# Optimization experiments

Hardware: AMD Instinct MI355X
Metric: run time of the kernel (lower is better)

Reference implementation:

```python
import jax, jax.numpy as jnp
import numpy as np

N_QUBITS = 9
N_LAYERS = 4
EPS = 1e-5


def _apply_ry(state, wire, theta):
    # state: [N, 2**n] real; theta: [N] or scalar
    n = N_QUBITS
    N = state.shape[0]
    left, right = 2 ** wire, 2 ** (n - 1 - wire)
    s = state.reshape(N, left, 2, right)
    th = jnp.broadcast_to(jnp.asarray(theta, state.dtype), (N,))[:, None, None]
    c, si = jnp.cos(th / 2), jnp.sin(th / 2)
    a, b = s[:, :, 0, :], s[:, :, 1, :]
    out = jnp.stack([c * a - si * b, si * a + c * b], axis=2)
    return out.reshape(N, -1)


def _apply_cnot(state, ctrl, tgt):
    n = N_QUBITS
    N = state.shape[0]
    s = state.reshape((N,) + (2,) * n)
    ca, ta = ctrl + 1, tgt + 1
    sub = jnp.take(s, 1, axis=ca)          # control == 1 slice
    ta2 = ta - 1 if ta > ca else ta
    sub = jnp.flip(sub, axis=ta2)          # X on target
    idx = [slice(None)] * (n + 1)
    idx[ca] = 1
    s = s.at[tuple(idx)].set(sub)
    return s.reshape(N, -1)


def quantum_layer(inputs, q_weights):
    # inputs: [N, n_qubits] angles; q_weights: [n_layers, n_qubits]
    N = inputs.shape[0]
    state = jnp.zeros((N, 2 ** N_QUBITS), inputs.dtype).at[:, 0].set(1.0)
    for i in range(N_QUBITS):
        state = _apply_ry(state, i, inputs[:, i])
    for j in range(N_LAYERS):
        for i in range(N_QUBITS):
            state = _apply_cnot(state, i, (i + 1) % N_QUBITS)
        for i in range(N_QUBITS):
            state = _apply_ry(state, i, q_weights[j, i])
    probs = (state * state).reshape((N,) + (2,) * N_QUBITS)
    zs = []
    for i in range(N_QUBITS):
        axes = tuple(a for a in range(1, N_QUBITS + 1) if a != i + 1)
        p = probs.sum(axes)                # [N, 2]
        zs.append(p[:, 0] - p[:, 1])
    return jnp.stack(zs, axis=1)           # [N, n_qubits]


def _bn(x):
    mu = x.mean((0, 2, 3), keepdims=True)
    var = x.var((0, 2, 3), keepdims=True)
    return (x - mu) * jax.lax.rsqrt(var + EPS)


def _maxpool(x, kh, kw):
    return jax.lax.reduce_window(x, -jnp.inf, jax.lax.max,
                                 (1, 1, kh, kw), (1, 1, kh, kw), 'VALID')


def _conv(x, w):
    return jax.lax.conv_general_dilated(x, w, (1, 1), 'VALID',
                                        dimension_numbers=('NCHW', 'OIHW', 'NCHW'))


def _forward(x, w_conv1, w_conv2, w_conv3, q_weights, fc_w, fc_b):
    h = jax.nn.elu(_bn(_conv(x, w_conv1)))
    h = jnp.pad(h, ((0, 0), (0, 0), (0, 1), (16, 17)))     # ZeroPad2d(16,17,0,1)
    h = _maxpool(jax.nn.elu(_bn(_conv(h, w_conv2))), 2, 4)
    h = jnp.pad(h, ((0, 0), (0, 0), (4, 3), (2, 1)))       # ZeroPad2d(2,1,4,3)
    h = _maxpool(jax.nn.elu(_bn(_conv(h, w_conv3))), 2, 4)
    B, C = h.shape[0], h.shape[1]
    feats = h.reshape(B, C, -1)                            # [B, 32, 9]
    q = quantum_layer(feats.reshape(B * C, N_QUBITS), q_weights)
    q = q.reshape(B, C * N_QUBITS)                         # channel-major concat
    return q @ fc_w.T + fc_b


def setup_inputs() -> dict:
    key = jax.random.key(0)
    ks = jax.random.split(key, 7)
    return {
        'x': jax.random.normal(ks[0], (1024, 1, 4, 216), jnp.float32),
        'w_conv1': jax.random.normal(ks[1], (16, 1, 1, 64), jnp.float32) * 0.05,
        'w_conv2': jax.random.normal(ks[2], (32, 16, 2, 32), jnp.float32) * 0.05,
        'w_conv3': jax.random.normal(ks[3], (32, 32, 8, 4), jnp.float32) * 0.05,
        'q_weights': jax.random.uniform(ks[4], (N_LAYERS, N_QUBITS), jnp.float32, 0.0, 2 * np.pi),
        'fc_w': jax.random.normal(ks[5], (5, 32 * N_QUBITS), jnp.float32) * 0.05,
        'fc_b': jnp.zeros((5,), jnp.float32),
    }


def reference(x, w_conv1, w_conv2, w_conv3, q_weights, fc_w, fc_b):
    return _forward(x, w_conv1, w_conv2, w_conv3, q_weights, fc_w, fc_b)
```

## Files before the change

### kernel.cpp

```cpp
#include <hip/hip_runtime.h>
#include <math.h>

#define NB 1024
#define C1 16
#define H1 4
#define W1 153
#define WX 216
#define K1 64
#define C2 32
#define H2 4
#define W2 155
#define W192 192
#define PW2 38
#define C3 32
#define W3 38

typedef short short4v __attribute__((ext_vector_type(4)));
typedef short short8 __attribute__((ext_vector_type(8)));
typedef float f32x16 __attribute__((ext_vector_type(16)));

#define OFF_OUT1     0
#define OFF_A1H      10027008
#define OFF_A1L      16318464
#define OFF_W2PH     22609920
#define OFF_W2PL     22626304
#define OFF_W3PH     22642688
#define OFF_W3PL     22659072
#define OFF_UH       22675456
#define OFF_UL       22806528
#define OFF_POOL2RAW 22937600
#define OFF_A2H      25427968
#define OFF_A2L      27787264
#define OFF_FEATSRAW 30146560
#define OFF_QO       30441472
#define OFF_PART1    30736384
#define OFF_PART2    30867456
#define OFF_PART3    30998528
#define OFF_STATS1   31031296
#define OFF_STATS2   31031328
#define OFF_STATS3   31031392

__device__ __forceinline__ float eluf(float x){ return x > 0.f ? x : expm1f(x); }

__device__ __forceinline__ ushort bf16h(float x){
  unsigned u = __float_as_uint(x);
  unsigned r = u + 0x7fffu + ((u >> 16) & 1u);
  return (ushort)(r >> 16);
}
__device__ __forceinline__ float bf16f(ushort h){ return __uint_as_float(((unsigned)h) << 16); }

__device__ __forceinline__ short8 cat8(short4v a, short4v b){
  return __builtin_shufflevector(a, b, 0,1,2,3,4,5,6,7);
}

__global__ __launch_bounds__(256) void k_conv1s(const float* __restrict__ x,
                                                const float* __restrict__ w1,
                                                float* __restrict__ out1,
                                                float* __restrict__ part1){
  __shared__ float xr[4][WX];
  __shared__ float wl[C1*K1];
  int n = blockIdx.x, tid = threadIdx.x;
  for (int i = tid; i < 4*WX; i += 256) xr[i/WX][i%WX] = x[(size_t)n*4*WX + i];
  for (int i = tid; i < C1*K1; i += 256) wl[i] = w1[i];
  __syncthreads();
  int h = tid >> 6, lane = tid & 63;
  float acc[16][3];
  #pragma unroll
  for (int c = 0; c < 16; ++c){ acc[c][0]=0.f; acc[c][1]=0.f; acc[c][2]=0.f; }
  bool v2 = (lane + 128) < W1;
  for (int k = 0; k < 64; ++k){
    float x0 = xr[h][lane + k];
    float x1 = xr[h][lane + 64 + k];
    float x2 = v2 ? xr[h][lane + 128 + k] : 0.f;
    #pragma unroll
    for (int c = 0; c < 16; ++c){
      float wk = wl[c*64 + k];
      acc[c][0] += wk*x0; acc[c][1] += wk*x1; acc[c][2] += wk*x2;
    }
  }
  float ss[16], sq[16];
  #pragma unroll
  for (int c = 0; c < 16; ++c){
    float* ob = out1 + (((size_t)(n*16 + c)*4 + h))*W1;
    ob[lane] = acc[c][0];
    ob[lane + 64] = acc[c][1];
    if (v2) ob[lane + 128] = acc[c][2];
    ss[c] = acc[c][0] + acc[c][1] + acc[c][2];
    sq[c] = acc[c][0]*acc[c][0] + acc[c][1]*acc[c][1] + acc[c][2]*acc[c][2];
  }
  #pragma unroll
  for (int m = 1; m < 64; m <<= 1){
    #pragma unroll
    for (int c = 0; c < 16; ++c){ ss[c] += __shfl_xor(ss[c], m); sq[c] += __shfl_xor(sq[c], m); }
  }
  if (lane == 0){
    #pragma unroll
    for (int c = 0; c < 16; ++c){
      part1[((size_t)(n*4 + h)*16 + c)*2]     = ss[c];
      part1[((size_t)(n*4 + h)*16 + c)*2 + 1] = sq[c];
    }
  }
}

__global__ __launch_bounds__(256) void k_stats_finP(const float* __restrict__ part,
                                                    float* __restrict__ stats,
                                                    int C, int nblk, float inv){
  __shared__ float rs[256], rq[256];
  int c = blockIdx.x;
  float s = 0.f, q = 0.f;
  for (int b = threadIdx.x; b < nblk; b += 256){
    s += part[((size_t)b*C + c)*2];
    q += part[((size_t)b*C + c)*2 + 1];
  }
  rs[threadIdx.x] = s; rq[threadIdx.x] = q; __syncthreads();
  for (int st = 128; st > 0; st >>= 1){
    if (threadIdx.x < st){ rs[threadIdx.x] += rs[threadIdx.x+st]; rq[threadIdx.x] += rq[threadIdx.x+st]; }
    __syncthreads();
  }
  if (threadIdx.x == 0){
    float mean = rs[0]*inv;
    float var  = rq[0]*inv - mean*mean;
    stats[c*2]   = mean;
    stats[c*2+1] = rsqrtf(var + 1e-5f);
  }
}

__global__ __launch_bounds__(256) void k_bnelu1(const float* __restrict__ out1,
                                                const float* __restrict__ stats,
                                                ushort* __restrict__ a1h, ushort* __restrict__ a1l){
  __shared__ float xf[2448];
  __shared__ float st[32];
  int b = blockIdx.x;
  int n = b >> 2, h = b & 3;
  int tid = threadIdx.x;
  if (tid < 32) st[tid] = stats[tid];
  for (int i = tid; i < 2448; i += 256){
    int ci = i / 153, w = i - ci*153;
    xf[i] = out1[((size_t)(n*16 + ci)*4 + h)*W1 + w];
  }
  __syncthreads();
  for (int i = tid; i < 3072; i += 256){
    int w = i >> 4, ci = i & 15;
    float v = 0.f;
    int ws = w - 16;
    if ((unsigned)ws < (unsigned)W1){
      float xx = xf[ci*153 + ws];
      v = eluf((xx - st[ci*2])*st[ci*2+1]);
    }
    int ciS = ci ^ (((w >> 2) & 3) << 2);
    size_t o = (size_t)b*3072 + w*16 + ciS;
    ushort hs = bf16h(v);
    a1h[o] = hs;
    a1l[o] = bf16h(v - bf16f(hs));
  }
}

__global__ void k_cvtw(const float* __restrict__ w2, const float* __restrict__ w3,
                       ushort* __restrict__ w2ph, ushort* __restrict__ w2pl,
                       ushort* __restrict__ w3ph, ushort* __restrict__ w3pl){
  int idx = blockIdx.x*256 + threadIdx.x;
  if (idx < 32768){
    int ci = idx & 15; int co = (idx >> 4) & 31; int rk = idx >> 9;
    int r = rk >> 5, kw = rk & 31;
    float v = w2[((size_t)(co*16 + ci)*2 + r)*32 + kw];
    ushort hs = bf16h(v); float hf = bf16f(hs);
    w2ph[idx] = hs; w2pl[idx] = bf16h(v - hf);
  } else {
    int j = idx - 32768;
    int ci = j & 31; int co = (j >> 5) & 31; int rk = j >> 10;
    int r = rk >> 2, kw = rk & 3;
    float v = w3[((size_t)(co*32 + ci)*8 + r)*4 + kw];
    ushort hs = bf16h(v); float hf = bf16f(hs);
    w3ph[j] = hs; w3pl[j] = bf16h(v - hf);
  }
}

template<int HG>
__global__ __launch_bounds__(256, 3) void k_conv2fT(const ushort* __restrict__ a1h,
                                                    const ushort* __restrict__ a1l,
                                                    const ushort* __restrict__ w2ph,
                                                    const ushort* __restrict__ w2pl,
                                                    float* __restrict__ pool2raw,
                                                    float* __restrict__ part2){
  constexpr int NR = HG ? 2 : 3;
  __shared__ __align__(16) ushort s_hi[NR*3072];
  __shared__ __align__(16) ushort s_lo[NR*3072];
  __shared__ float statW[4][32][2];
  int n = blockIdx.x;
  int tid = threadIdx.x;
  {
    const float4* gh = (const float4*)(a1h + ((size_t)n*4 + 2*HG)*3072);
    const float4* gl = (const float4*)(a1l + ((size_t)n*4 + 2*HG)*3072);
    float4* dh = (float4*)s_hi;
    float4* dl = (float4*)s_lo;
    #pragma unroll
    for (int i = 0; i < NR*384; i += 256){
      int k = i + tid;
      if (k < NR*384){ dh[k] = gh[k]; dl[k] = gl[k]; }
    }
  }
  __syncthreads();
  int wv = tid >> 6, lane = tid & 63;
  int l5 = lane >> 5, l31 = lane & 31;
  int ps = (wv + n) & 3;
  int p0 = (ps == 0) ? 0 : (ps + 1);
  bool two = (ps == 0);
  int e4 = l5*4;

  f32x16 acc[2][2];
  #pragma unroll
  for (int lh = 0; lh < 2; ++lh)
    #pragma unroll
    for (int p = 0; p < 2; ++p)
      #pragma unroll
      for (int e = 0; e < 16; ++e) acc[lh][p][e] = 0.f;

  for (int kw = 0; kw < 32; ++kw){
    short8 Ah[2], Al[2];
    #pragma unroll
    for (int r = 0; r < 2; ++r){
      int widx = ((r*32 + kw)*32 + l31)*16 + e4;
      Ah[r] = cat8(*(const short4v*)(w2ph + widx), *(const short4v*)(w2ph + widx + 8));
      Al[r] = cat8(*(const short4v*)(w2pl + widx), *(const short4v*)(w2pl + widx + 8));
    }
    short8 bh[NR][2], bl[NR][2];
    #pragma unroll
    for (int j = 0; j < NR; ++j){
      #pragma unroll
      for (int p = 0; p < 2; ++p){
        int pf = p0 + p; pf = (pf > 4) ? 4 : pf;
        int pos = pf*32 + l31 + kw;
        int sw = ((pos >> 2) & 3) << 2;
        int off0 = j*3072 + pos*16 + (e4 ^ sw);
        int off1 = off0 ^ 8;
        bh[j][p] = cat8(*(const short4v*)(s_hi + off0), *(const short4v*)(s_hi + off1));
        bl[j][p] = cat8(*(const short4v*)(s_lo + off0), *(const short4v*)(s_lo + off1));
      }
    }
    #pragma unroll
    for (int lh = 0; lh < 2; ++lh){
      #pragma unroll
      for (int r = 0; r < 2; ++r){
        if (lh + r < NR){
          acc[lh][0] = __builtin_amdgcn_mfma_f32_32x32x16_bf16(Ah[r], bh[lh+r][0], acc[lh][0], 0, 0, 0);
          acc[lh][0] = __builtin_amdgcn_mfma_f32_32x32x16_bf16(Ah[r], bl[lh+r][0], acc[lh][0], 0, 0, 0);
          acc[lh][0] = __builtin_amdgcn_mfma_f32_32x32x16_bf16(Al[r], bh[lh+r][0], acc[lh][0], 0, 0, 0);
        }
      }
    }
    if (two){
      #pragma unroll
      for (int lh = 0; lh < 2; ++lh){
        #pragma unroll
        for (int r = 0; r < 2; ++r){
          if (lh + r < NR){
            acc[lh][1] = __builtin_amdgcn_mfma_f32_32x32x16_bf16(Ah[r], bh[lh+r][1], acc[lh][1], 0, 0, 0);
            acc[lh][1] = __builtin_amdgcn_mfma_f32_32x32x16_bf16(Ah[r], bl[lh+r][1], acc[lh][1], 0, 0, 0);
            acc[lh][1] = __builtin_amdgcn_mfma_f32_32x32x16_bf16(Al[r], bh[lh+r][1], acc[lh][1], 0, 0, 0);
          }
        }
      }
    }
  }

  int np = two ? 2 : 1;
  {
    float sreg[16], qreg[16];
    #pragma unroll
    for (int e = 0; e < 16; ++e){ sreg[e] = 0.f; qreg[e] = 0.f; }
    #pragma unroll
    for (int lh = 0; lh < 2; ++lh){
      #pragma unroll
      for (int p = 0; p < 2; ++p){
        bool pv = (p < np) && (((p0 + p) < 4) || (l31 < 27));
        #pragma unroll
        for (int e = 0; e < 16; ++e){
          float v = pv ? acc[lh][p][e] : 0.f;
          sreg[e] += v; qreg[e] += v*v;
        }
      }
    }
    #pragma unroll
    for (int m = 1; m < 32; m <<= 1){
      #pragma unroll
      for (int e = 0; e < 16; ++e){
        sreg[e] += __shfl_xor(sreg[e], m);
        qreg[e] += __shfl_xor(qreg[e], m);
      }
    }
    if (l31 == 0){
      #pragma unroll
      for (int e = 0; e < 16; ++e){
        int co = (e & 3) + ((e >> 2) << 3) + (l5 << 2);
        statW[ps][co][0] = sreg[e];
        statW[ps][co][1] = qreg[e];
      }
    }
  }
  #pragma unroll
  for (int p = 0; p < 2; ++p){
    if (p < np){
      #pragma unroll
      for (int e = 0; e < 16; ++e){
        float m0 = fmaxf(acc[0][p][e], acc[1][p][e]);
        float v1 = fmaxf(m0, __shfl_xor(m0, 1));
        float v2m = fmaxf(v1, __shfl_xor(v1, 2));
        int pw = (p0 + p)*8 + (l31 >> 2);
        if ((l31 & 3) == 0 && pw < PW2){
          int co = (e & 3) + ((e >> 2) << 3) + (l5 << 2);
          pool2raw[(((size_t)n*2 + HG)*32 + co)*PW2 + pw] = v2m;
        }
      }
    }
  }
  __syncthreads();
  if (tid < 32){
    float s = statW[0][tid][0] + statW[1][tid][0] + statW[2][tid][0] + statW[3][tid][0];
    float q = statW[0][tid][1] + statW[1][tid][1] + statW[2][tid][1] + statW[3][tid][1];
    part2[(((size_t)n*2 + HG)*32 + tid)*2]     = s;
    part2[(((size_t)n*2 + HG)*32 + tid)*2 + 1] = q;
  }
}

__global__ __launch_bounds__(256) void k_bn2(const float* __restrict__ pool2raw,
                                             const float* __restrict__ stats,
                                             ushort* __restrict__ a2h, ushort* __restrict__ a2l){
  __shared__ float xf[1216];
  __shared__ float st[64];
  int b = blockIdx.x;
  int tid = threadIdx.x;
  if (tid < 64) st[tid] = stats[tid];
  for (int i = tid; i < 1216; i += 256) xf[i] = pool2raw[(size_t)b*1216 + i];
  __syncthreads();
  for (int i = tid; i < 2304; i += 256){
    int w = i >> 5, ci = i & 31;
    float v = 0.f;
    int pw = w - 2;
    if ((unsigned)pw < (unsigned)PW2)
      v = eluf((xf[ci*38 + pw] - st[ci*2])*st[ci*2+1]);
    int ciS = ci ^ (((w >> 1) & 7) << 2);
    size_t o = (size_t)b*2304 + w*32 + ciS;
    ushort hs = bf16h(v);
    a2h[o] = hs; a2l[o] = bf16h(v - bf16f(hs));
  }
}

__global__ __launch_bounds__(256, 2) void k_conv3f(const ushort* __restrict__ a2h,
                                                   const ushort* __restrict__ a2l,
                                                   const ushort* __restrict__ w3ph,
                                                   const ushort* __restrict__ w3pl,
                                                   float* __restrict__ featsraw,
                                                   float* __restrict__ part3){
  __shared__ __align__(16) ushort s3h[9216];
  __shared__ __align__(16) ushort s3l[9216];
  __shared__ float poolL3[4][32][12];
  __shared__ float statL3[4][32][2];
  int nb = blockIdx.x;
  int tid = threadIdx.x;
  {
    const float4* gh = (const float4*)(a2h + (size_t)nb*9216);
    const float4* gl = (const float4*)(a2l + (size_t)nb*9216);
    float4* dh = (float4*)s3h;
    float4* dl = (float4*)s3l;
    for (int i = tid; i < 1152; i += 256){ dh[i] = gh[i]; dl[i] = gl[i]; }
  }
  __syncthreads();
  int wave = tid >> 6, lane = tid & 63;
  int nh = wave >> 1, h = wave & 1;
  int l5 = lane >> 5, l31 = lane & 31;

  f32x16 acc[2];
  #pragma unroll
  for (int p = 0; p < 2; ++p)
    #pragma unroll
    for (int e = 0; e < 16; ++e) acc[p][e] = 0.f;

  #pragma unroll
  for (int ri = 0; ri < 2; ++ri){
    int r = (h == 0) ? (4 + ri) : (3 + ri);
    int rbase = (nh*2 + ri)*72*32;
    #pragma unroll
    for (int kw = 0; kw < 4; ++kw){
      #pragma unroll
      for (int ch = 0; ch < 2; ++ch){
        int widx = ((r*4 + kw)*32 + l31)*32 + ch*16 + l5*4;
        short8 Ah = cat8(*(const short4v*)(w3ph + widx), *(const short4v*)(w3ph + widx + 8));
        short8 Al = cat8(*(const short4v*)(w3pl + widx), *(const short4v*)(w3pl + widx + 8));
        short8 Bh[2], Bl[2];
        #pragma unroll
        for (int p = 0; p < 2; ++p){
          int pos = p*32 + l31 + kw;
          int sw = ((pos >> 1) & 7) << 2;
          int s0 = ch*16 + l5*4;
          int off0 = rbase + pos*32 + (s0 ^ sw);
          int off1 = rbase + pos*32 + ((s0 + 8) ^ sw);
          Bh[p] = cat8(*(const short4v*)(s3h + off0), *(const short4v*)(s3h + off1));
          Bl[p] = cat8(*(const short4v*)(s3l + off0), *(const short4v*)(s3l + off1));
        }
        #pragma unroll
        for (int p = 0; p < 2; ++p) acc[p] = __builtin_amdgcn_mfma_f32_32x32x16_bf16(Ah, Bh[p], acc[p], 0, 0, 0);
        #pragma unroll
        for (int p = 0; p < 2; ++p) acc[p] = __builtin_amdgcn_mfma_f32_32x32x16_bf16(Ah, Bl[p], acc[p], 0, 0, 0);
        #pragma unroll
        for (int p = 0; p < 2; ++p) acc[p] = __builtin_amdgcn_mfma_f32_32x32x16_bf16(Al, Bh[p], acc[p], 0, 0, 0);
      }
    }
  }

  {
    float sreg[16], qreg[16];
    #pragma unroll
    for (int e = 0; e < 16; ++e){ sreg[e] = 0.f; qreg[e] = 0.f; }
    #pragma unroll
    for (int p = 0; p < 2; ++p){
      bool pv = (p == 0) || (l31 < 6);
      #pragma unroll
      for (int e = 0; e < 16; ++e){
        float v = pv ? acc[p][e] : 0.f;
        sreg[e] += v; qreg[e] += v*v;
      }
    }
    #pragma unroll
    for (int m = 1; m < 32; m <<= 1){
      #pragma unroll
      for (int e = 0; e < 16; ++e){
        sreg[e] += __shfl_xor(sreg[e], m);
        qreg[e] += __shfl_xor(qreg[e], m);
      }
    }
    if (l31 == 0){
      #pragma unroll
      for (int e = 0; e < 16; ++e){
        int co = (e & 3) + ((e >> 2) << 3) + (l5 << 2);
        statL3[wave][co][0] = sreg[e];
        statL3[wave][co][1] = qreg[e];
      }
    }
  }
  #pragma unroll
  for (int p = 0; p < 2; ++p){
    #pragma unroll
    for (int e = 0; e < 16; ++e){
      float v = acc[p][e];
      float v1 = fmaxf(v, __shfl_xor(v, 1));
      float v2m = fmaxf(v1, __shfl_xor(v1, 2));
      int pw = p*8 + (l31 >> 2);
      if ((l31 & 3) == 0 && pw < 9){
        int co = (e & 3) + ((e >> 2) << 3) + (l5 << 2);
        poolL3[wave][co][pw] = v2m;
      }
    }
  }
  __syncthreads();
  for (int i = tid; i < 2*32*9; i += 256){
    int pw = i % 9; int t = i / 9; int co = t & 31; int nh2 = t >> 5;
    float v = fmaxf(poolL3[nh2*2][co][pw], poolL3[nh2*2+1][co][pw]);
    featsraw[((size_t)(nb*2 + nh2)*32 + co)*9 + pw] = v;
  }
  if (tid < 32){
    float s = 0.f, q = 0.f;
    #pragma unroll
    for (int wv = 0; wv < 4; ++wv){ s += statL3[wv][tid][0]; q += statL3[wv][tid][1]; }
    part3[((size_t)nb*32 + tid)*2]     = s;
    part3[((size_t)nb*32 + tid)*2 + 1] = q;
  }
}

__global__ __launch_bounds__(256) void k_buildU(const float* __restrict__ qw,
                                                ushort* __restrict__ Uh, ushort* __restrict__ Ul){
  __shared__ float wt[36][2];
  int tid = threadIdx.x;
  if (tid < 36){ float s, c; sincosf(qw[tid]*0.5f, &s, &c); wt[tid][0] = c; wt[tid][1] = s; }
  __syncthreads();
  int wid = tid >> 6, lane = tid & 63;
  int k = blockIdx.x*4 + wid;
  float v[8];
  #pragma unroll
  for (int r = 0; r < 8; ++r) v[r] = (lane*8 + r == k) ? 1.f : 0.f;

  for (int j = 0; j < 4; ++j){
    #pragma unroll
    for (int i = 0; i < 5; ++i){
      int cm = 32>>i, tm = 16>>i;
      bool flip = (lane & cm) != 0;
      #pragma unroll
      for (int r = 0; r < 8; ++r){
        float w = __shfl_xor(v[r], tm);
        v[r] = flip ? w : v[r];
      }
    }
    { bool flip = (lane & 1) != 0;
      #pragma unroll
      for (int r = 0; r < 4; ++r){ float a = v[r], bb = v[r+4]; v[r] = flip?bb:a; v[r+4] = flip?a:bb; } }
    { float t = v[4]; v[4] = v[6]; v[6] = t; t = v[5]; v[5] = v[7]; v[7] = t; }
    { float t = v[2]; v[2] = v[3]; v[3] = t; t = v[6]; v[6] = v[7]; v[7] = t; }
    #pragma unroll
    for (int r = 1; r < 8; r += 2) v[r] = __shfl_xor(v[r], 32);

    #pragma unroll
    for (int i = 0; i < 6; ++i){
      float c = wt[j*9+i][0], s = wt[j*9+i][1];
      int m = 32>>i;
      float sg = (lane & m) ? s : -s;
      #pragma unroll
      for (int r = 0; r < 8; ++r){
        float w = __shfl_xor(v[r], m);
        v[r] = c*v[r] + sg*w;
      }
    }
    { float c = wt[j*9+6][0], s = wt[j*9+6][1];
      #pragma unroll
      for (int r = 0; r < 4; ++r){ float a = v[r], bb = v[r+4]; v[r] = c*a - s*bb; v[r+4] = s*a + c*bb; } }
    { float c = wt[j*9+7][0], s = wt[j*9+7][1]; float a, bb;
      a=v[0]; bb=v[2]; v[0]=c*a-s*bb; v[2]=s*a+c*bb;
      a=v[1]; bb=v[3]; v[1]=c*a-s*bb; v[3]=s*a+c*bb;
      a=v[4]; bb=v[6]; v[4]=c*a-s*bb; v[6]=s*a+c*bb;
      a=v[5]; bb=v[7]; v[5]=c*a-s*bb; v[7]=s*a+c*bb; }
    { float c = wt[j*9+8][0], s = wt[j*9+8][1]; float a, bb;
      a=v[0]; bb=v[1]; v[0]=c*a-s*bb; v[1]=s*a+c*bb;
      a=v[2]; bb=v[3]; v[2]=c*a-s*bb; v[3]=s*a+c*bb;
      a=v[4]; bb=v[5]; v[4]=c*a-s*bb; v[5]=s*a+c*bb;
      a=v[6]; bb=v[7]; v[6]=c*a-s*bb; v[7]=s*a+c*bb; }
  }
  #pragma unroll
  for (int r = 0; r < 8; ++r){
    int s = lane*8 + r;
    int mf = s >> 5, r31 = s & 31;
    int addr = (((k >> 4)*16 + mf)*32 + r31)*16 + (k & 15);
    float f = v[r];
    ushort hi = bf16h(f);
    Uh[addr] = hi;
    Ul[addr] = bf16h(f - bf16f(hi));
  }
}

__global__ __launch_bounds__(256, 1) void k_qgemm(const float* __restrict__ featsraw,
                                                  const float* __restrict__ stats,
                                                  const ushort* __restrict__ Uh,
                                                  const ushort* __restrict__ Ul,
                                                  float* __restrict__ qo){
  __shared__ __align__(16) ushort BhL[32768];
  __shared__ __align__(16) ushort BlL[32768];
  __shared__ float angL[576];
  __shared__ float zred[4][64][9];
  int nb = blockIdx.x;
  int tid = threadIdx.x;
  for (int t = tid; t < 576; t += 256){
    float vr = featsraw[(size_t)nb*576 + t];
    int c = (t/9) & 31;
    angL[t] = 0.5f * eluf((vr - stats[c*2])*stats[c*2+1]);
  }
  __syncthreads();
  {
    int sm = tid >> 2, q = tid & 3;
    float tc[9], ts[9];
    #pragma unroll
    for (int i = 0; i < 9; ++i) sincosf(angL[sm*9 + i], &ts[i], &tc[i]);
    float Pc = ((q & 2) ? ts[0] : tc[0]) * ((q & 1) ? ts[1] : tc[1]);
    int swz = (sm >> 2) & 3;
    short4v* bh4 = (short4v*)BhL;
    short4v* bl4 = (short4v*)BlL;
    int j = 0;
    #pragma unroll
    for (int b2 = 0; b2 < 2; ++b2){ float p2 = Pc*(b2 ? ts[2] : tc[2]);
    #pragma unroll
    for (int b3 = 0; b3 < 2; ++b3){ float p3 = p2*(b3 ? ts[3] : tc[3]);
    #pragma unroll
    for (int b4 = 0; b4 < 2; ++b4){ float p4 = p3*(b4 ? ts[4] : tc[4]);
    #pragma unroll
    for (int b5 = 0; b5 < 2; ++b5){ float p5 = p4*(b5 ? ts[5] : tc[5]);
    #pragma unroll
    for (int b6 = 0; b6 < 2; ++b6){ float p6 = p5*(b6 ? ts[6] : tc[6]);
      float a0 = p6*tc[7]*tc[8];
      float a1 = p6*tc[7]*ts[8];
      float a2 = p6*ts[7]*tc[8];
      float a3 = p6*ts[7]*ts[8];
      ushort h0 = bf16h(a0), h1 = bf16h(a1), h2 = bf16h(a2), h3 = bf16h(a3);
      short4v hv; hv[0]=(short)h0; hv[1]=(short)h1; hv[2]=(short)h2; hv[3]=(short)h3;
      short4v lv; lv[0]=(short)bf16h(a0 - bf16f(h0)); lv[1]=(short)bf16h(a1 - bf16f(h1));
                  lv[2]=(short)bf16h(a2 - bf16f(h2)); lv[3]=(short)bf16h(a3 - bf16f(h3));
      int kk = q*128 + j;
      int kstep = kk >> 4;
      int g = (kk >> 2) & 3;
      int idx4 = (kstep*64 + sm)*4 + (g ^ swz);
      bh4[idx4] = hv; bl4[idx4] = lv;
      j += 4;
    }}}}}
  }
  __syncthreads();
  int wv = tid >> 6, lane = tid & 63, l5 = lane >> 5, l31 = lane & 31;
  f32x16 acc[4][2];
  #pragma unroll
  for (int jj = 0; jj < 4; ++jj)
    #pragma unroll
    for (int nf = 0; nf < 2; ++nf)
      #pragma unroll
      for (int e = 0; e < 16; ++e) acc[jj][nf][e] = 0.f;

  for (int kstep = 0; kstep < 32; ++kstep){
    short8 Bh[2], Bl[2];
    #pragma unroll
    for (int nf = 0; nf < 2; ++nf){
      int sm = nf*32 + l31;
      int base = (kstep*64 + sm)*16;
      int sz = ((sm >> 2) & 3) << 2;
      int e0 = (l5*4) ^ sz;
      int e1 = (l5*4 + 8) ^ sz;
      Bh[nf] = cat8(*(const short4v*)(BhL + base + e0), *(const short4v*)(BhL + base + e1));
      Bl[nf] = cat8(*(const short4v*)(BlL + base + e0), *(const short4v*)(BlL + base + e1));
    }
    #pragma unroll
    for (int jj = 0; jj < 4; ++jj){
      int mf = wv*4 + jj;
      const ushort* ah = Uh + ((kstep*16 + mf)*32 + l31)*16 + l5*4;
      const ushort* al = Ul + ((kstep*16 + mf)*32 + l31)*16 + l5*4;
      short8 Ah = cat8(*(const short4v*)ah, *(const short4v*)(ah + 8));
      short8 Al = cat8(*(const short4v*)al, *(const short4v*)(al + 8));
      acc[jj][0] = __builtin_amdgcn_mfma_f32_32x32x16_bf16(Ah, Bh[0], acc[jj][0], 0, 0, 0);
      acc[jj][1] = __builtin_amdgcn_mfma_f32_32x32x16_bf16(Ah, Bh[1], acc[jj][1], 0, 0, 0);
      acc[jj][0] = __builtin_amdgcn_mfma_f32_32x32x16_bf16(Ah, Bl[0], acc[jj][0], 0, 0, 0);
      acc[jj][1] = __builtin_amdgcn_mfma_f32_32x32x16_bf16(Ah, Bl[1], acc[jj][1], 0, 0, 0);
      acc[jj][0] = __builtin_amdgcn_mfma_f32_32x32x16_bf16(Al, Bh[0], acc[jj][0], 0, 0, 0);
      acc[jj][1] = __builtin_amdgcn_mfma_f32_32x32x16_bf16(Al, Bh[1], acc[jj][1], 0, 0, 0);
    }
  }
  float zz[2][9];
  #pragma unroll
  for (int nf = 0; nf < 2; ++nf)
    #pragma unroll
    for (int i = 0; i < 9; ++i) zz[nf][i] = 0.f;
  #pragma unroll
  for (int jj = 0; jj < 4; ++jj){
    int mf = wv*4 + jj;
    float sg0 = (mf & 8) ? -1.f : 1.f;
    float sg1 = (mf & 4) ? -1.f : 1.f;
    float sg2 = (mf & 2) ? -1.f : 1.f;
    float sg3 = (mf & 1) ? -1.f : 1.f;
    #pragma unroll
    for (int nf = 0; nf < 2; ++nf){
      float psum = 0.f, z4 = 0.f, z5 = 0.f, z7 = 0.f, z8 = 0.f;
      #pragma unroll
      for (int e = 0; e < 16; ++e){
        float qv = acc[jj][nf][e]*acc[jj][nf][e];
        psum += qv;
        z4 += ((e >> 3) & 1) ? -qv : qv;
        z5 += ((e >> 2) & 1) ? -qv : qv;
        z7 += ((e >> 1) & 1) ? -qv : qv;
        z8 += (e & 1) ? -qv : qv;
      }
      zz[nf][0] += sg0*psum; zz[nf][1] += sg1*psum;
      zz[nf][2] += sg2*psum; zz[nf][3] += sg3*psum;
      zz[nf][4] += z4; zz[nf][5] += z5;
      zz[nf][6] += l5 ? -psum : psum;
      zz[nf][7] += z7; zz[nf][8] += z8;
    }
  }
  #pragma unroll
  for (int nf = 0; nf < 2; ++nf)
    #pragma unroll
    for (int i = 0; i < 9; ++i) zz[nf][i] += __shfl_xor(zz[nf][i], 32);
  if (l5 == 0){
    #pragma unroll
    for (int nf = 0; nf < 2; ++nf)
      #pragma unroll
      for (int i = 0; i < 9; ++i) zred[wv][nf*32 + l31][i] = zz[nf][i];
  }
  __syncthreads();
  for (int t = tid; t < 576; t += 256){
    int sm = t / 9, i = t - sm*9;
    float s = zred[0][sm][i] + zred[1][sm][i] + zred[2][sm][i] + zred[3][sm][i];
    qo[(size_t)(nb*64 + sm)*9 + i] = s;
  }
}

__global__ void k_fc(const float* __restrict__ q, const float* __restrict__ fw,
                     const float* __restrict__ fb, float* __restrict__ out){
  int idx = blockIdx.x*256 + threadIdx.x;
  if (idx >= NB*5) return;
  int b = idx / 5, o = idx - b*5;
  const float* qr = q + (size_t)b*288;
  const float* wr = fw + (size_t)o*288;
  float s = 0.f;
  for (int j = 0; j < 288; ++j) s += qr[j]*wr[j];
  out[idx] = s + fb[o];
}

extern "C" void kernel_launch(void* const* d_in, const int* in_sizes, int n_in,
                              void* d_out, int out_size, void* d_ws, size_t ws_size,
                              hipStream_t stream){
  const float* x  = (const float*)d_in[0];
  const float* w1 = (const float*)d_in[1];
  const float* w2 = (const float*)d_in[2];
  const float* w3 = (const float*)d_in[3];
  const float* qw = (const float*)d_in[4];
  const float* fw = (const float*)d_in[5];
  const float* fb = (const float*)d_in[6];
  float* out = (float*)d_out;
  float* W = (float*)d_ws;

  float*  out1   = W + OFF_OUT1;
  ushort* a1h    = (ushort*)(W + OFF_A1H);
  ushort* a1l    = (ushort*)(W + OFF_A1L);
  ushort* w2ph   = (ushort*)(W + OFF_W2PH);
  ushort* w2pl   = (ushort*)(W + OFF_W2PL);
  ushort* w3ph   = (ushort*)(W + OFF_W3PH);
  ushort* w3pl   = (ushort*)(W + OFF_W3PL);
  ushort* uH     = (ushort*)(W + OFF_UH);
  ushort* uL     = (ushort*)(W + OFF_UL);
  float*  pool2raw = W + OFF_POOL2RAW;
  ushort* a2h    = (ushort*)(W + OFF_A2H);
  ushort* a2l    = (ushort*)(W + OFF_A2L);
  float*  featsraw = W + OFF_FEATSRAW;
  float*  qo     = W + OFF_QO;
  float*  part1  = W + OFF_PART1;
  float*  part2  = W + OFF_PART2;
  float*  part3  = W + OFF_PART3;
  float*  stats1 = W + OFF_STATS1;
  float*  stats2 = W + OFF_STATS2;
  float*  stats3 = W + OFF_STATS3;

  k_conv1s<<<NB, 256, 0, stream>>>(x, w1, out1, part1);
  k_stats_finP<<<16, 256, 0, stream>>>(part1, stats1, 16, NB*4, 1.f/((float)NB*H1*W1));
  k_bnelu1<<<NB*4, 256, 0, stream>>>(out1, stats1, a1h, a1l);
  k_cvtw<<<256, 256, 0, stream>>>(w2, w3, w2ph, w2pl, w3ph, w3pl);
  k_buildU<<<128, 256, 0, stream>>>(qw, uH, uL);
  k_conv2fT<0><<<NB, 256, 0, stream>>>(a1h, a1l, w2ph, w2pl, pool2raw, part2);
  k_conv2fT<1><<<NB, 256, 0, stream>>>(a1h, a1l, w2ph, w2pl, pool2raw, part2);
  k_stats_finP<<<32, 256, 0, stream>>>(part2, stats2, 32, NB*2, 1.f/((float)NB*H2*W2));
  k_bn2<<<NB*2, 256, 0, stream>>>(pool2raw, stats2, a2h, a2l);
  k_conv3f<<<NB/2, 256, 0, stream>>>(a2h, a2l, w3ph, w3pl, featsraw, part3);
  k_stats_finP<<<32, 256, 0, stream>>>(part3, stats3, 32, NB/2, 1.f/((float)NB*2*W3));
  k_qgemm<<<NB/2, 256, 0, stream>>>(featsraw, stats3, uH, uL, qo);
  k_fc<<<20, 256, 0, stream>>>(qo, fw, fb, out);
}
```

Baseline: 337.9 us.

## Split conv2 work across five waves, one position tile per wave

The conv2 kernel moves from 4 waves per block, where one wave handled two position tiles, to 5 waves of 320 threads, each handling exactly one 32-wide position tile. This removes the imbalance in which one wave did double the MFMA work while the others idled. Launch bounds change to (320,5), and the per-wave stats array grows to five slots. The cost is more waves per block and a possible change in register budget and occupancy.

Result: faster. 328.2 us (-2.9%).

```diff
diff --git a/kernel.cpp b/kernel.cpp
--- a/kernel.cpp
+++ b/kernel.cpp
@@ -176,7 +176,7 @@
 }
 
 template<int HG>
-__global__ __launch_bounds__(256, 3) void k_conv2fT(const ushort* __restrict__ a1h,
+__global__ __launch_bounds__(320, 5) void k_conv2f5(const ushort* __restrict__ a1h,
                                                     const ushort* __restrict__ a1l,
                                                     const ushort* __restrict__ w2ph,
                                                     const ushort* __restrict__ w2pl,
@@ -185,7 +185,7 @@
   constexpr int NR = HG ? 2 : 3;
   __shared__ __align__(16) ushort s_hi[NR*3072];
   __shared__ __align__(16) ushort s_lo[NR*3072];
-  __shared__ float statW[4][32][2];
+  __shared__ float statW[5][32][2];
   int n = blockIdx.x;
   int tid = threadIdx.x;
   {
@@ -193,27 +193,17 @@
     const float4* gl = (const float4*)(a1l + ((size_t)n*4 + 2*HG)*3072);
     float4* dh = (float4*)s_hi;
     float4* dl = (float4*)s_lo;
-    #pragma unroll
-    for (int i = 0; i < NR*384; i += 256){
-      int k = i + tid;
-      if (k < NR*384){ dh[k] = gh[k]; dl[k] = gl[k]; }
-    }
-  }
-  __syncthreads();
-  int wv = tid >> 6, lane = tid & 63;
+    for (int i = tid; i < NR*384; i += 320){ dh[i] = gh[i]; dl[i] = gl[i]; }
+  }
+  __syncthreads();
+  int wave = tid >> 6, lane = tid & 63;
   int l5 = lane >> 5, l31 = lane & 31;
-  int ps = (wv + n) & 3;
-  int p0 = (ps == 0) ? 0 : (ps + 1);
-  bool two = (ps == 0);
+  int p = wave + (n % 5); p = (p >= 5) ? p - 5 : p;
   int e4 = l5*4;
 
-  f32x16 acc[2][2];
-  #pragma unroll
-  for (int lh = 0; lh < 2; ++lh)
-    #pragma unroll
-    for (int p = 0; p < 2; ++p)
-      #pragma unroll
-      for (int e = 0; e < 16; ++e) acc[lh][p][e] = 0.f;
+  f32x16 acc0, acc1;
+  #pragma unroll
+  for (int e = 0; e < 16; ++e){ acc0[e] = 0.f; acc1[e] = 0.f; }
 
   for (int kw = 0; kw < 32; ++kw){
     short8 Ah[2], Al[2];
@@ -223,62 +213,41 @@
       Ah[r] = cat8(*(const short4v*)(w2ph + widx), *(const short4v*)(w2ph + widx + 8));
       Al[r] = cat8(*(const short4v*)(w2pl + widx), *(const short4v*)(w2pl + widx + 8));
     }
-    short8 bh[NR][2], bl[NR][2];
+    short8 bh[NR], bl[NR];
+    int pos = p*32 + l31 + kw;
+    int sw = ((pos >> 2) & 3) << 2;
+    int o0 = pos*16 + (e4 ^ sw);
     #pragma unroll
     for (int j = 0; j < NR; ++j){
-      #pragma unroll
-      for (int p = 0; p < 2; ++p){
-        int pf = p0 + p; pf = (pf > 4) ? 4 : pf;
-        int pos = pf*32 + l31 + kw;
-        int sw = ((pos >> 2) & 3) << 2;
-        int off0 = j*3072 + pos*16 + (e4 ^ sw);
-        int off1 = off0 ^ 8;
-        bh[j][p] = cat8(*(const short4v*)(s_hi + off0), *(const short4v*)(s_hi + off1));
-        bl[j][p] = cat8(*(const short4v*)(s_lo + off0), *(const short4v*)(s_lo + off1));
-      }
-    }
-    #pragma unroll
-    for (int lh = 0; lh < 2; ++lh){
-      #pragma unroll
-      for (int r = 0; r < 2; ++r){
-        if (lh + r < NR){
-          acc[lh][0] = __builtin_amdgcn_mfma_f32_32x32x16_bf16(Ah[r], bh[lh+r][0], acc[lh][0], 0, 0, 0);
-          acc[lh][0] = __builtin_amdgcn_mfma_f32_32x32x16_bf16(Ah[r], bl[lh+r][0], acc[lh][0], 0, 0, 0);
-          acc[lh][0] = __builtin_amdgcn_mfma_f32_32x32x16_bf16(Al[r], bh[lh+r][0], acc[lh][0], 0, 0, 0);
-        }
-      }
-    }
-    if (two){
-      #pragma unroll
-      for (int lh = 0; lh < 2; ++lh){
-        #pragma unroll
-        for (int r = 0; r < 2; ++r){
-          if (lh + r < NR){
-            acc[lh][1] = __builtin_amdgcn_mfma_f32_32x32x16_bf16(Ah[r], bh[lh+r][1], acc[lh][1], 0, 0, 0);
-            acc[lh][1] = __builtin_amdgcn_mfma_f32_32x32x16_bf16(Ah[r], bl[lh+r][1], acc[lh][1], 0, 0, 0);
-            acc[lh][1] = __builtin_amdgcn_mfma_f32_32x32x16_bf16(Al[r], bh[lh+r][1], acc[lh][1], 0, 0, 0);
-          }
-        }
-      }
-    }
-  }
-
-  int np = two ? 2 : 1;
+      int off = j*3072 + o0;
+      bh[j] = cat8(*(const short4v*)(s_hi + off), *(const short4v*)(s_hi + (off ^ 8)));
+      bl[j] = cat8(*(const short4v*)(s_lo + off), *(const short4v*)(s_lo + (off ^ 8)));
+    }
+    acc0 = __builtin_amdgcn_mfma_f32_32x32x16_bf16(Ah[0], bh[0], acc0, 0, 0, 0);
+    acc0 = __builtin_amdgcn_mfma_f32_32x32x16_bf16(Ah[0], bl[0], acc0, 0, 0, 0);
+    acc0 = __builtin_amdgcn_mfma_f32_32x32x16_bf16(Al[0], bh[0], acc0, 0, 0, 0);
+    acc0 = __builtin_amdgcn_mfma_f32_32x32x16_bf16(Ah[1], bh[1], acc0, 0, 0, 0);
+    acc0 = __builtin_amdgcn_mfma_f32_32x32x16_bf16(Ah[1], bl[1], acc0, 0, 0, 0);
+    acc0 = __builtin_amdgcn_mfma_f32_32x32x16_bf16(Al[1], bh[1], acc0, 0, 0, 0);
+    acc1 = __builtin_amdgcn_mfma_f32_32x32x16_bf16(Ah[0], bh[1], acc1, 0, 0, 0);
+    acc1 = __builtin_amdgcn_mfma_f32_32x32x16_bf16(Ah[0], bl[1], acc1, 0, 0, 0);
+    acc1 = __builtin_amdgcn_mfma_f32_32x32x16_bf16(Al[0], bh[1], acc1, 0, 0, 0);
+    if constexpr (NR == 3){
+      acc1 = __builtin_amdgcn_mfma_f32_32x32x16_bf16(Ah[1], bh[2], acc1, 0, 0, 0);
+      acc1 = __builtin_amdgcn_mfma_f32_32x32x16_bf16(Ah[1], bl[2], acc1, 0, 0, 0);
+      acc1 = __builtin_amdgcn_mfma_f32_32x32x16_bf16(Al[1], bh[2], acc1, 0, 0, 0);
+    }
+  }
+
   {
     float sreg[16], qreg[16];
-    #pragma unroll
-    for (int e = 0; e < 16; ++e){ sreg[e] = 0.f; qreg[e] = 0.f; }
-    #pragma unroll
-    for (int lh = 0; lh < 2; ++lh){
-      #pragma unroll
-      for (int p = 0; p < 2; ++p){
-        bool pv = (p < np) && (((p0 + p) < 4) || (l31 < 27));
-        #pragma unroll
-        for (int e = 0; e < 16; ++e){
-          float v = pv ? acc[lh][p][e] : 0.f;
-          sreg[e] += v; qreg[e] += v*v;
-        }
-      }
+    bool pv = (p < 4) || (l31 < 27);
+    #pragma unroll
+    for (int e = 0; e < 16; ++e){
+      float v0 = pv ? acc0[e] : 0.f;
+      float v1 = pv ? acc1[e] : 0.f;
+      sreg[e] = v0 + v1;
+      qreg[e] = v0*v0 + v1*v1;
     }
     #pragma unroll
     for (int m = 1; m < 32; m <<= 1){
@@ -292,31 +261,26 @@
       #pragma unroll
       for (int e = 0; e < 16; ++e){
         int co = (e & 3) + ((e >> 2) << 3) + (l5 << 2);
-        statW[ps][co][0] = sreg[e];
-        statW[ps][co][1] = qreg[e];
-      }
-    }
-  }
-  #pragma unroll
-  for (int p = 0; p < 2; ++p){
-    if (p < np){
-      #pragma unroll
-      for (int e = 0; e < 16; ++e){
-        float m0 = fmaxf(acc[0][p][e], acc[1][p][e]);
-        float v1 = fmaxf(m0, __shfl_xor(m0, 1));
-        float v2m = fmaxf(v1, __shfl_xor(v1, 2));
-        int pw = (p0 + p)*8 + (l31 >> 2);
-        if ((l31 & 3) == 0 && pw < PW2){
-          int co = (e & 3) + ((e >> 2) << 3) + (l5 << 2);
-          pool2raw[(((size_t)n*2 + HG)*32 + co)*PW2 + pw] = v2m;
-        }
-      }
+        statW[p][co][0] = sreg[e];
+        statW[p][co][1] = qreg[e];
+      }
+    }
+  }
+  #pragma unroll
+  for (int e = 0; e < 16; ++e){
+    float m0 = fmaxf(acc0[e], acc1[e]);
+    float v1 = fmaxf(m0, __shfl_xor(m0, 1));
+    float v2m = fmaxf(v1, __shfl_xor(v1, 2));
+    int pw = p*8 + (l31 >> 2);
+    if ((l31 & 3) == 0 && pw < PW2){
+      int co = (e & 3) + ((e >> 2) << 3) + (l5 << 2);
+      pool2raw[(((size_t)n*2 + HG)*32 + co)*PW2 + pw] = v2m;
     }
   }
   __syncthreads();
   if (tid < 32){
-    float s = statW[0][tid][0] + statW[1][tid][0] + statW[2][tid][0] + statW[3][tid][0];
-    float q = statW[0][tid][1] + statW[1][tid][1] + statW[2][tid][1] + statW[3][tid][1];
+    float s = statW[0][tid][0] + statW[1][tid][0] + statW[2][tid][0] + statW[3][tid][0] + statW[4][tid][0];
+    float q = statW[0][tid][1] + statW[1][tid][1] + statW[2][tid][1] + statW[3][tid][1] + statW[4][tid][1];
     part2[(((size_t)n*2 + HG)*32 + tid)*2]     = s;
     part2[(((size_t)n*2 + HG)*32 + tid)*2 + 1] = q;
   }
@@ -724,8 +688,8 @@
   k_bnelu1<<<NB*4, 256, 0, stream>>>(out1, stats1, a1h, a1l);
   k_cvtw<<<256, 256, 0, stream>>>(w2, w3, w2ph, w2pl, w3ph, w3pl);
   k_buildU<<<128, 256, 0, stream>>>(qw, uH, uL);
-  k_conv2fT<0><<<NB, 256, 0, stream>>>(a1h, a1l, w2ph, w2pl, pool2raw, part2);
-  k_conv2fT<1><<<NB, 256, 0, stream>>>(a1h, a1l, w2ph, w2pl, pool2raw, part2);
+  k_conv2f5<0><<<NB, 320, 0, stream>>>(a1h, a1l, w2ph, w2pl, pool2raw, part2);
+  k_conv2f5<1><<<NB, 320, 0, stream>>>(a1h, a1l, w2ph, w2pl, pool2raw, part2);
   k_stats_finP<<<32, 256, 0, stream>>>(part2, stats2, 32, NB*2, 1.f/((float)NB*H2*W2));
   k_bn2<<<NB*2, 256, 0, stream>>>(pool2raw, stats2, a2h, a2l);
   k_conv3f<<<NB/2, 256, 0, stream>>>(a2h, a2l, w3ph, w3pl, featsraw, part3);
```
